# Kernel tuning notes

Hardware: AMD Instinct MI355X
Metric: run time of the kernel (lower is better)

The kernel has to match this reference:

```python
import jax, jax.numpy as jnp
import numpy as np

B, F, FO, J, H, IN, OUT = 256, 16, 32, 22, 8, 256, 512
HID = OUT // H    # 64
HS = HID // 2     # 32 (spatial/temporal half)
NEG = -1e9


def setup_inputs() -> dict:
    key = jax.random.key(0)
    ks = jax.random.split(key, 10)
    s = 0.02
    f32 = jnp.float32
    return {
        "q": jax.random.normal(ks[0], (B, FO, J, IN), f32),
        "k": jax.random.normal(ks[1], (B, F, J, IN), f32),
        "v": jax.random.normal(ks[2], (B, F, J, IN), f32),
        "mask_s": jax.random.randint(ks[3], (J, J), 0, 2, jnp.int32),
        "mask_t": jax.random.randint(ks[4], (FO, FO), 0, 2, jnp.int32),
        "Wq_w": jax.random.normal(ks[5], (IN, OUT), f32) * s,
        "Wq_b": jnp.zeros((OUT,), f32),
        "Wk_w": jax.random.normal(ks[6], (IN, OUT), f32) * s,
        "Wk_b": jnp.zeros((OUT,), f32),
        "Wv_w": jax.random.normal(ks[7], (IN, OUT), f32) * s,
        "Wv_b": jnp.zeros((OUT,), f32),
        "conv_s_w": jax.random.normal(ks[8], (FO, F), f32) * s,  # 1x1 Conv2d over frame channels
        "conv_s_b": jnp.zeros((FO,), f32),
        "conv_t_w": jax.random.normal(ks[9], (FO, F), f32) * s,
        "conv_t_b": jnp.zeros((FO,), f32),
    }


def _forward(q, k, v, mask_s, mask_t, Wq_w, Wq_b, Wk_w, Wk_b, Wv_w, Wv_b,
             conv_s_w, conv_s_b, conv_t_w, conv_t_b):
    b = q.shape[0]
    temporal_size = q.shape[1]  # torch: q.shape[1] AFTER Wq -> num_frames_out
    q = q @ Wq_w + Wq_b
    k = k @ Wk_w + Wk_b
    v = v @ Wv_w + Wv_b
    # raw reshapes, exactly as the torch module (not a standard head split)
    q = q.reshape(b, H, FO, J, HID)
    k = k.reshape(b, H, F, J, HID)
    v = v.reshape(b, H, F, J, HID)
    q_s, q_t = q[..., :HS], q[..., HS:]
    k_s, k_t = k[..., :HS], k[..., HS:]
    v_s, v_t = v[..., :HS], v[..., HS:]

    def explode_s(x):
        # (b,H,F,J,HS) -> merge heads into channels -> 1x1 conv over frames -> (b,H,FO,J,HS)
        x = x.transpose(0, 2, 3, 1, 4).reshape(b, F, J, H * HS)
        x = jnp.einsum('of,bfjc->bojc', conv_s_w, x) + conv_s_b[None, :, None, None]
        return x.reshape(b, FO, J, H, HS).transpose(0, 3, 1, 2, 4)

    k_s = explode_s(k_s)
    v_s = explode_s(v_s)

    q_t = q_t.transpose(0, 1, 3, 2, 4)  # (b,H,J,FO,HS)
    v_t = v_t.transpose(0, 1, 3, 2, 4)  # (b,H,J,F,HS)
    kt = k_t.reshape(b * H, F, J, HS)   # torch double-permute is identity
    kt = jnp.einsum('of,nfjc->nojc', conv_t_w, kt) + conv_t_b[None, :, None, None]
    k_t = kt.reshape(b, H, FO, J, HS).transpose(0, 1, 3, 2, 4)  # (b,H,J,FO,HS)

    # faithful to torch.einsum: no shared contraction index -> outer product of sums
    attn_s = jnp.einsum('bhtsc,bhtdu->bhtsu', q_s, jnp.swapaxes(k_s, 3, 4))  # (b,H,FO,J,J)
    attn_s = jnp.where(mask_s == 0, NEG, attn_s)
    attn_t = jnp.einsum('bhstf,bhsug->bhstg', q_t, jnp.swapaxes(k_t, 3, 4))  # (b,H,J,FO,FO)
    attn_t = jnp.where(mask_t == 0, NEG, attn_t)
    attn_s = jax.nn.softmax(attn_s, axis=-1)
    attn_t = jax.nn.softmax(attn_t, axis=-1)

    # 'bhtss' takes the diagonal over the two joint axes (torch semantics)
    x_s = jnp.einsum('bhtss,bhtuf->bhtsf', attn_s, v_s)          # (b,H,FO,J,HS)
    x_t = jnp.einsum('bhstf,bhsug->bhstg', attn_t, v_t)          # (b,H,J,FO,HS)
    x_t = x_t.transpose(0, 1, 3, 2, 4)                            # (b,H,FO,J,HS)

    x_up = jnp.concatenate([x_s[:, :, :temporal_size], x_t], axis=-1)
    x_after_s = x_s[:, :, temporal_size:]                         # empty when q covers FO frames
    x_after = jnp.concatenate([x_after_s, jnp.zeros_like(x_after_s)], axis=-1)
    x = jnp.concatenate([x_up, x_after], axis=2)
    x = x.transpose(0, 2, 3, 1, 4).reshape(b, FO, J, H * HID)
    return x


def reference(q, k, v, mask_s, mask_t, Wq_w, Wq_b, Wk_w, Wk_b, Wv_w, Wv_b,
              conv_s_w, conv_s_b, conv_t_w, conv_t_b):
    return _forward(q, k, v, mask_s, mask_t, Wq_w, Wq_b, Wk_w, Wk_b, Wv_w, Wv_b,
                    conv_s_w, conv_s_b, conv_t_w, conv_t_b)
```

## Files before the change

kernel.cpp:

```cpp
#include <hip/hip_runtime.h>


#define NEGV (-1000000000.0f)

typedef __attribute__((ext_vector_type(8))) short short8;
typedef __attribute__((ext_vector_type(4))) float f32x4;

__device__ inline ushort f2bf(float f) {
  union { float f; unsigned u; } a;
  a.f = f;
  unsigned u = a.u;
  return (ushort)((u + 0x7FFFu + ((u >> 16) & 1u)) >> 16);
}

#define PUTG(g, pa, pb)                                                        \
  {                                                                            \
    int row_ = (g) >> 5, gl_ = (g) & 31;                                       \
    int gp_ = gl_ ^ (row_ & 7);                                                \
    short8 u_;                                                                 \
    u_[0] = (short)f2bf(pa[0]); u_[1] = (short)f2bf(pa[1]);                    \
    u_[2] = (short)f2bf(pa[2]); u_[3] = (short)f2bf(pa[3]);                    \
    u_[4] = (short)f2bf(pb[0]); u_[5] = (short)f2bf(pb[1]);                    \
    u_[6] = (short)f2bf(pb[2]); u_[7] = (short)f2bf(pb[3]);                    \
    *reinterpret_cast<short8*>(&lA[row_ * 256 + gp_ * 8]) = u_;                \
  }

#define STAGE44_NT(SRCPTR)                                                     \
  {                                                                            \
    const float* vsrc_ = (SRCPTR);                                             \
    int g0 = tid, g1 = tid + 512, g2 = tid + 1024;                             \
    f32x4 a0 = __builtin_nontemporal_load(                                     \
        reinterpret_cast<const f32x4*>(vsrc_ + g0 * 8));                       \
    f32x4 b0 = __builtin_nontemporal_load(                                     \
        reinterpret_cast<const f32x4*>(vsrc_ + g0 * 8 + 4));                   \
    f32x4 a1 = __builtin_nontemporal_load(                                     \
        reinterpret_cast<const f32x4*>(vsrc_ + g1 * 8));                       \
    f32x4 b1 = __builtin_nontemporal_load(                                     \
        reinterpret_cast<const f32x4*>(vsrc_ + g1 * 8 + 4));                   \
    f32x4 a2 = {0, 0, 0, 0}, b2 = {0, 0, 0, 0};                                \
    if (g2 < 1408) {                                                           \
      a2 = __builtin_nontemporal_load(                                         \
          reinterpret_cast<const f32x4*>(vsrc_ + g2 * 8));                     \
      b2 = __builtin_nontemporal_load(                                         \
          reinterpret_cast<const f32x4*>(vsrc_ + g2 * 8 + 4));                 \
    }                                                                          \
    PUTG(g0, a0, b0);                                                          \
    PUTG(g1, a1, b1);                                                          \
    if (g2 < 1408) PUTG(g2, a2, b2);                                           \
    if (tid < 128) {                                                           \
      int g = 1408 + tid;                                                      \
      int row_ = g >> 5, gp_ = (g & 31) ^ (row_ & 7);                          \
      short8 z = {0, 0, 0, 0, 0, 0, 0, 0};                                     \
      *reinterpret_cast<short8*>(&lA[row_ * 256 + gp_ * 8]) = z;               \
    }                                                                          \
  }

__global__ __launch_bounds__(512) void prep_all_kernel(const float* __restrict__ Wq_w,
                                                       const float* __restrict__ Wq_b,
                                                       const float* __restrict__ Wk_w,
                                                       const float* __restrict__ Wk_b,
                                                       const float* __restrict__ Wv_w,
                                                       ushort* __restrict__ qwf,
                                                       ushort* __restrict__ kwf,
                                                       ushort* __restrict__ wvtf,
                                                       float* __restrict__ sqb,
                                                       float* __restrict__ skb) {
  int bx = blockIdx.x, tid = threadIdx.x;
  if (bx < 256) {
    int idx = bx * 512 + tid;
    int e = idx & 7;
    int lane = (idx >> 3) & 63;
    int ks = (idx >> 9) & 7;
    int nt = idx >> 12;
    int r0 = lane & 15, kb = lane >> 4;
    int k = ks * 32 + kb * 8 + e;
    int ch = nt * 16 + r0;
    wvtf[idx] = f2bf(Wv_w[k * 512 + ch]);
  } else if (bx < 272) {
    int idx = (bx - 256) * 512 + tid;
    int which = idx >> 12;
    int r = idx & 4095;
    int e = r & 7;
    int lane = (r >> 3) & 63;
    int ks = r >> 9;
    int m = lane & 15, kb = lane >> 4;
    int k = ks * 32 + kb * 8 + e;
    float s = 0.f;
    if (m < 8) {
      const float* W = which ? Wk_w : Wq_w;
      const float4* p = reinterpret_cast<const float4*>(W + (size_t)k * 512 + m * 64);
      #pragma unroll
      for (int c4 = 0; c4 < 8; ++c4) {
        float4 x = p[c4];
        s += x.x + x.y + x.z + x.w;
      }
    }
    (which ? kwf : qwf)[r] = f2bf(s);
  } else {
    if (tid < 8) {
      float s = 0.f;
      for (int c = 0; c < 32; ++c) s += Wq_b[tid * 64 + c];
      sqb[tid] = s;
    } else if (tid < 16) {
      int mm = tid - 8;
      float s = 0.f;
      for (int c = 0; c < 32; ++c) s += Wk_b[mm * 64 + c];
      skb[mm] = s;
    }
  }
}

__global__ __launch_bounds__(512, 2) void mega_kernel(const float* __restrict__ q,
                                                      const float* __restrict__ k,
                                                      const float* __restrict__ v,
                                                      const ushort* __restrict__ qwf,
                                                      const ushort* __restrict__ kwf,
                                                      const ushort* __restrict__ wvtf,
                                                      const float* __restrict__ sqb,
                                                      const float* __restrict__ skb,
                                                      const float* __restrict__ Wv_b,
                                                      const float* __restrict__ csw,
                                                      const float* __restrict__ csb,
                                                      const int* __restrict__ mask_s,
                                                      float* __restrict__ out) {
  int bh = blockIdx.x;
  int b = bh >> 3, h = bh & 7;
  __shared__ float sbuf[6656];
  __shared__ float qs[32][23];
  __shared__ float kraw[16][23];
  __shared__ float vsg[16][33];
  __shared__ float vtl[22][33];
  __shared__ float lcsw[32][17];
  __shared__ int msk[484];
  ushort* lA = reinterpret_cast<ushort*>(sbuf);
  float* dump = sbuf;
  float* kssp = sbuf;
  float* vssp = sbuf + 736;
  float* dgp = sbuf + 1792;
  int tid = threadIdx.x, lane = tid & 63, w = tid >> 6;
  int r0 = lane & 15, kb = lane >> 4;

  STAGE44_NT(v + (size_t)bh * 11264);

  if (tid < 484) msk[tid] = mask_s[tid];
  {
    int t = tid >> 4, f = tid & 15;
    lcsw[t][f] = csw[t * 16 + f];
  }
  if (tid < 32) lcsw[tid][16] = csb[tid];

  const float* qbase = q + (size_t)(b * 704 + 4 * h * 22) * 256;
  const float* kbase = k + (size_t)(b * 352 + 2 * h * 22) * 256;
  for (int pass = 0; pass < 2; ++pass) {
    int u = pass == 0 ? w : 8;
    if (pass == 1 && w != 0) break;
    bool isK = u >= 6;
    int ut = isK ? u - 6 : u;
    int limit = isK ? 44 : 88;
    int rr = ut * 16 + r0;
    if (rr >= limit) rr = 0;
    const float* src = (isK ? kbase : qbase) + (size_t)rr * 256;
    const ushort* wf = isK ? kwf : qwf;
    f32x4 acc = {0.f, 0.f, 0.f, 0.f};
    #pragma unroll
    for (int ks = 0; ks < 8; ++ks) {
      f32x4 xa = __builtin_nontemporal_load(
          reinterpret_cast<const f32x4*>(src + ks * 32 + kb * 8));
      f32x4 xb = __builtin_nontemporal_load(
          reinterpret_cast<const f32x4*>(src + ks * 32 + kb * 8 + 4));
      short8 a;
      a[0] = (short)f2bf(xa[0]); a[1] = (short)f2bf(xa[1]);
      a[2] = (short)f2bf(xa[2]); a[3] = (short)f2bf(xa[3]);
      a[4] = (short)f2bf(xb[0]); a[5] = (short)f2bf(xb[1]);
      a[6] = (short)f2bf(xb[2]); a[7] = (short)f2bf(xb[3]);
      short8 bf = *reinterpret_cast<const short8*>(wf + (ks * 64 + lane) * 8);
      acc = __builtin_amdgcn_mfma_f32_16x16x32_bf16(a, bf, acc, 0, 0, 0);
    }
    if (r0 < 8) {
      int m = r0;
      float bias = isK ? skb[m] : sqb[m];
      #pragma unroll
      for (int reg = 0; reg < 4; ++reg) {
        int R = ut * 16 + kb * 4 + reg;
        if (R < limit) {
          if (!isK) {
            int fo2l = R / 22, j2 = R % 22;
            int lf = fo2l * 11264 + j2 * 512 + m * 64;
            int t = lf / 1408;
            int s = (lf % 1408) >> 6;
            qs[t][s] = acc[reg] + bias;
          } else {
            int f2l = R / 22, j2 = R % 22;
            int lf = f2l * 11264 + j2 * 512 + m * 64;
            int floc = lf / 1408;
            int jj = (lf % 1408) >> 6;
            kraw[floc][jj] = acc[reg] + bias;
          }
        }
      }
    }
  }
  __syncthreads();

  int nt0 = w * 4;
  f32x4 acc[3][4];
  #pragma unroll
  for (int m = 0; m < 3; ++m)
    #pragma unroll
    for (int n = 0; n < 4; ++n) acc[m][n] = (f32x4){0.f, 0.f, 0.f, 0.f};

  #pragma unroll
  for (int ks = 0; ks < 8; ++ks) {
    int go = ((ks * 4 + kb) ^ (r0 & 7)) * 8;
    short8 a0 = *reinterpret_cast<const short8*>(&lA[(r0) * 256 + go]);
    short8 a1 = *reinterpret_cast<const short8*>(&lA[(16 + r0) * 256 + go]);
    short8 a2 = *reinterpret_cast<const short8*>(&lA[(32 + r0) * 256 + go]);
    #pragma unroll
    for (int n = 0; n < 4; ++n) {
      short8 bf = *reinterpret_cast<const short8*>(
          wvtf + ((size_t)((nt0 + n) * 8 + ks) * 64 + lane) * 8);
      acc[0][n] = __builtin_amdgcn_mfma_f32_16x16x32_bf16(bf, a0, acc[0][n], 0, 0, 0);
      acc[1][n] = __builtin_amdgcn_mfma_f32_16x16x32_bf16(bf, a1, acc[1][n], 0, 0, 0);
      acc[2][n] = __builtin_amdgcn_mfma_f32_16x16x32_bf16(bf, a2, acc[2][n], 0, 0, 0);
    }
  }
  __syncthreads();

  #pragma unroll
  for (int n = 0; n < 4; ++n) {
    float4 bq = *reinterpret_cast<const float4*>(Wv_b + w * 64 + n * 16 + kb * 4);
    int dbase = tid * 13;
    #pragma unroll
    for (int m = 0; m < 3; ++m) {
      dump[dbase + m * 4 + 0] = acc[m][n][0] + bq.x;
      dump[dbase + m * 4 + 1] = acc[m][n][1] + bq.y;
      dump[dbase + m * 4 + 2] = acc[m][n][2] + bq.z;
      dump[dbase + m * 4 + 3] = acc[m][n][3] + bq.w;
    }
    __syncthreads();
    if (n < 2) {
      if (tid < 256) {
        int f = tid >> 4, rest = tid & 15;
        int kb2 = rest >> 2, reg = rest & 3;
        float s = 0.f;
        #pragma unroll
        for (int u = 0; u < 22; ++u) {
          int fj = f * 22 + u;
          int f2 = (fj >= 176) ? 1 : 0;
          int rem = fj - f2 * 176;
          int j = rem >> 3, ww = rem & 7;
          int vrow = f2 * 22 + j;
          int m = vrow >> 4, rr2 = vrow & 15;
          s += dump[(ww * 64 + kb2 * 16 + rr2) * 13 + m * 4 + reg];
        }
        vsg[f][n * 16 + kb2 * 4 + reg] = s;
      }
    } else {
      if (tid < 352) {
        int jj = tid >> 4, rest = tid & 15;
        int kb2 = rest >> 2, reg = rest & 3;
        float s = 0.f;
        #pragma unroll
        for (int f = 0; f < 16; ++f) {
          int fj = f * 22 + jj;
          int f2 = (fj >= 176) ? 1 : 0;
          int rem = fj - f2 * 176;
          int j = rem >> 3, ww = rem & 7;
          int vrow = f2 * 22 + j;
          int m = vrow >> 4, rr2 = vrow & 15;
          s += dump[(ww * 64 + kb2 * 16 + rr2) * 13 + m * 4 + reg];
        }
        vtl[jj][(n - 2) * 16 + kb2 * 4 + reg] = s;
      }
    }
    __syncthreads();
  }

  float* ob = out + (size_t)b * 32 * 22 * 512 + h * 64;
  for (int i = tid; i < 5632; i += 512) {
    int ts = i >> 3, w4 = i & 7;
    int t = ts / 22, s = ts % 22;
    int d0 = 32 + w4 * 4;
    const float* tp = &vtl[s][d0 - 32];
    f32x4 val = {tp[0], tp[1], tp[2], tp[3]};
    *reinterpret_cast<f32x4*>(ob + (size_t)(t * 22 + s) * 512 + d0) = val;
  }

  for (int o = tid; o < 704; o += 512) {
    int t = o / 22, j = o % 22;
    float a = 32.0f * lcsw[t][16];
    #pragma unroll
    for (int f = 0; f < 16; ++f) a += lcsw[t][f] * kraw[f][j];
    kssp[t * 23 + j] = a;
  }
  {
    int t = tid >> 4, d2 = (tid & 15) * 2;
    float a0 = 22.0f * lcsw[t][16], a1 = a0;
    #pragma unroll
    for (int f = 0; f < 16; ++f) {
      float cw = lcsw[t][f];
      a0 += cw * vsg[f][d2];
      a1 += cw * vsg[f][d2 + 1];
    }
    vssp[t * 33 + d2] = a0;
    vssp[t * 33 + d2 + 1] = a1;
  }
  __syncthreads();

  for (int p = tid; p < 704; p += 512) {
    int t = p / 22, s = p % 22;
    float qv = qs[t][s];
    float mx = -3.0e38f;
    #pragma unroll
    for (int u = 0; u < 22; ++u) {
      float av = msk[s * 22 + u] ? qv * kssp[t * 23 + u] : NEGV;
      mx = fmaxf(mx, av);
    }
    float den = 0.f;
    #pragma unroll
    for (int u = 0; u < 22; ++u) {
      float av = msk[s * 22 + u] ? qv * kssp[t * 23 + u] : NEGV;
      den += expf(av - mx);
    }
    float as = msk[s * 22 + s] ? qv * kssp[t * 23 + s] : NEGV;
    dgp[t * 23 + s] = expf(as - mx) / den;
  }
  __syncthreads();

  for (int i = tid; i < 5632; i += 512) {
    int ts = i >> 3, w4 = i & 7;
    int t = ts / 22, s = ts % 22;
    int d0 = w4 * 4;
    float g = dgp[t * 23 + s];
    const float* vp = &vssp[t * 33 + d0];
    f32x4 val = {g * vp[0], g * vp[1], g * vp[2], g * vp[3]};
    *reinterpret_cast<f32x4*>(ob + (size_t)(t * 22 + s) * 512 + d0) = val;
  }
}

extern "C" void kernel_launch(void* const* d_in, const int* in_sizes, int n_in,
                              void* d_out, int out_size, void* d_ws, size_t ws_size,
                              hipStream_t stream) {
  const float* q = (const float*)d_in[0];
  const float* k = (const float*)d_in[1];
  const float* v = (const float*)d_in[2];
  const int* mask_s = (const int*)d_in[3];
  const float* Wq_w = (const float*)d_in[5];
  const float* Wq_b = (const float*)d_in[6];
  const float* Wk_w = (const float*)d_in[7];
  const float* Wk_b = (const float*)d_in[8];
  const float* Wv_w = (const float*)d_in[9];
  const float* Wv_b = (const float*)d_in[10];
  const float* csw = (const float*)d_in[11];
  const float* csb = (const float*)d_in[12];
  float* out = (float*)d_out;

  float* ws = (float*)d_ws;
  float* sqb = ws;
  float* skb = ws + 8;
  ushort* wvtf = (ushort*)(ws + 16);
  ushort* qwf = (ushort*)(ws + 65552);
  ushort* kwf = (ushort*)(ws + 67600);

  hipLaunchKernelGGL(prep_all_kernel, dim3(273), dim3(512), 0, stream,
                     Wq_w, Wq_b, Wk_w, Wk_b, Wv_w, qwf, kwf, wvtf, sqb, skb);
  hipLaunchKernelGGL(mega_kernel, dim3(2048), dim3(512), 0, stream,
                     q, k, v, qwf, kwf, wvtf, sqb, skb, Wv_b, csw, csb, mask_s, out);
}
```

Baseline: 187.7 us.

## Split V-projection MFMA into two column passes and restructure LDS reduction dump

```diff
diff --git a/kernel.cpp b/kernel.cpp
--- a/kernel.cpp
+++ b/kernel.cpp
@@ -125,24 +125,23 @@
                                                       float* __restrict__ out) {
   int bh = blockIdx.x;
   int b = bh >> 3, h = bh & 7;
-  __shared__ float sbuf[6656];
+  __shared__ ushort lA[48 * 256];
+  __shared__ float dmp[4096];
   __shared__ float qs[32][23];
   __shared__ float kraw[16][23];
   __shared__ float vsg[16][33];
   __shared__ float vtl[22][33];
   __shared__ float lcsw[32][17];
-  __shared__ int msk[484];
-  ushort* lA = reinterpret_cast<ushort*>(sbuf);
-  float* dump = sbuf;
-  float* kssp = sbuf;
-  float* vssp = sbuf + 736;
-  float* dgp = sbuf + 1792;
+  __shared__ char msk[484];
+  float* kssp = dmp;
+  float* vssp = dmp + 736;
+  float* dgp = dmp + 1792;
   int tid = threadIdx.x, lane = tid & 63, w = tid >> 6;
   int r0 = lane & 15, kb = lane >> 4;
 
   STAGE44_NT(v + (size_t)bh * 11264);
 
-  if (tid < 484) msk[tid] = mask_s[tid];
+  if (tid < 484) msk[tid] = (char)mask_s[tid];
   {
     int t = tid >> 4, f = tid & 15;
     lcsw[t][f] = csw[t * 16 + f];
@@ -203,78 +202,105 @@
   __syncthreads();
 
   int nt0 = w * 4;
-  f32x4 acc[3][4];
   #pragma unroll
-  for (int m = 0; m < 3; ++m)
-    #pragma unroll
-    for (int n = 0; n < 4; ++n) acc[m][n] = (f32x4){0.f, 0.f, 0.f, 0.f};
-
-  #pragma unroll
-  for (int ks = 0; ks < 8; ++ks) {
-    int go = ((ks * 4 + kb) ^ (r0 & 7)) * 8;
-    short8 a0 = *reinterpret_cast<const short8*>(&lA[(r0) * 256 + go]);
-    short8 a1 = *reinterpret_cast<const short8*>(&lA[(16 + r0) * 256 + go]);
-    short8 a2 = *reinterpret_cast<const short8*>(&lA[(32 + r0) * 256 + go]);
-    #pragma unroll
-    for (int n = 0; n < 4; ++n) {
-      short8 bf = *reinterpret_cast<const short8*>(
-          wvtf + ((size_t)((nt0 + n) * 8 + ks) * 64 + lane) * 8);
-      acc[0][n] = __builtin_amdgcn_mfma_f32_16x16x32_bf16(bf, a0, acc[0][n], 0, 0, 0);
-      acc[1][n] = __builtin_amdgcn_mfma_f32_16x16x32_bf16(bf, a1, acc[1][n], 0, 0, 0);
-      acc[2][n] = __builtin_amdgcn_mfma_f32_16x16x32_bf16(bf, a2, acc[2][n], 0, 0, 0);
+  for (int r = 0; r < 2; ++r) {
+    f32x4 acc[3][2];
+    #pragma unroll
+    for (int m = 0; m < 3; ++m)
+      #pragma unroll
+      for (int nl = 0; nl < 2; ++nl) acc[m][nl] = (f32x4){0.f, 0.f, 0.f, 0.f};
+
+    #pragma unroll
+    for (int ks = 0; ks < 8; ++ks) {
+      int go = ((ks * 4 + kb) ^ (r0 & 7)) * 8;
+      short8 a0 = *reinterpret_cast<const short8*>(&lA[(r0) * 256 + go]);
+      short8 a1 = *reinterpret_cast<const short8*>(&lA[(16 + r0) * 256 + go]);
+      short8 a2 = *reinterpret_cast<const short8*>(&lA[(32 + r0) * 256 + go]);
+      #pragma unroll
+      for (int nl = 0; nl < 2; ++nl) {
+        short8 bf = *reinterpret_cast<const short8*>(
+            wvtf + ((size_t)((nt0 + r * 2 + nl) * 8 + ks) * 64 + lane) * 8);
+        acc[0][nl] = __builtin_amdgcn_mfma_f32_16x16x32_bf16(bf, a0, acc[0][nl], 0, 0, 0);
+        acc[1][nl] = __builtin_amdgcn_mfma_f32_16x16x32_bf16(bf, a1, acc[1][nl], 0, 0, 0);
+        acc[2][nl] = __builtin_amdgcn_mfma_f32_16x16x32_bf16(bf, a2, acc[2][nl], 0, 0, 0);
+      }
+    }
+
+    #pragma unroll
+    for (int nl = 0; nl < 2; ++nl) {
+      int n = r * 2 + nl;
+      float4 bq = *reinterpret_cast<const float4*>(Wv_b + w * 64 + n * 16 + kb * 4);
+      #pragma unroll
+      for (int msub = 0; msub < 2; ++msub) {
+        __syncthreads();
+        if (msub == 0) {
+          #pragma unroll
+          for (int m = 0; m < 2; ++m) {
+            dmp[(m * 4 + 0) * 512 + tid] = acc[m][nl][0] + bq.x;
+            dmp[(m * 4 + 1) * 512 + tid] = acc[m][nl][1] + bq.y;
+            dmp[(m * 4 + 2) * 512 + tid] = acc[m][nl][2] + bq.z;
+            dmp[(m * 4 + 3) * 512 + tid] = acc[m][nl][3] + bq.w;
+          }
+        } else {
+          dmp[0 * 512 + tid] = acc[2][nl][0] + bq.x;
+          dmp[1 * 512 + tid] = acc[2][nl][1] + bq.y;
+          dmp[2 * 512 + tid] = acc[2][nl][2] + bq.z;
+          dmp[3 * 512 + tid] = acc[2][nl][3] + bq.w;
+        }
+        __syncthreads();
+        if (n < 2) {
+          if (tid < 256) {
+            int f = tid >> 4, rest = tid & 15;
+            int kb2 = rest >> 2, reg = rest & 3;
+            float s = 0.f;
+            #pragma unroll
+            for (int u = 0; u < 22; ++u) {
+              int fj = f * 22 + u;
+              int f2 = (fj >= 176) ? 1 : 0;
+              int rem = fj - f2 * 176;
+              int j = rem >> 3, ww = rem & 7;
+              int vrow = f2 * 22 + j;
+              int m = vrow >> 4, rr2 = vrow & 15;
+              int src = ww * 64 + kb2 * 16 + rr2;
+              if (msub == 0) {
+                if (m < 2) s += dmp[(m * 4 + reg) * 512 + src];
+              } else {
+                if (m == 2) s += dmp[reg * 512 + src];
+              }
+            }
+            int d = n * 16 + kb2 * 4 + reg;
+            if (msub == 0) vsg[f][d] = s;
+            else vsg[f][d] += s;
+          }
+        } else {
+          if (tid < 352) {
+            int jj = tid >> 4, rest = tid & 15;
+            int kb2 = rest >> 2, reg = rest & 3;
+            float s = 0.f;
+            #pragma unroll
+            for (int f = 0; f < 16; ++f) {
+              int fj = f * 22 + jj;
+              int f2 = (fj >= 176) ? 1 : 0;
+              int rem = fj - f2 * 176;
+              int j = rem >> 3, ww = rem & 7;
+              int vrow = f2 * 22 + j;
+              int m = vrow >> 4, rr2 = vrow & 15;
+              int src = ww * 64 + kb2 * 16 + rr2;
+              if (msub == 0) {
+                if (m < 2) s += dmp[(m * 4 + reg) * 512 + src];
+              } else {
+                if (m == 2) s += dmp[reg * 512 + src];
+              }
+            }
+            int g = (n - 2) * 16 + kb2 * 4 + reg;
+            if (msub == 0) vtl[jj][g] = s;
+            else vtl[jj][g] += s;
+          }
+        }
+      }
     }
   }
   __syncthreads();
-
-  #pragma unroll
-  for (int n = 0; n < 4; ++n) {
-    float4 bq = *reinterpret_cast<const float4*>(Wv_b + w * 64 + n * 16 + kb * 4);
-    int dbase = tid * 13;
-    #pragma unroll
-    for (int m = 0; m < 3; ++m) {
-      dump[dbase + m * 4 + 0] = acc[m][n][0] + bq.x;
-      dump[dbase + m * 4 + 1] = acc[m][n][1] + bq.y;
-      dump[dbase + m * 4 + 2] = acc[m][n][2] + bq.z;
-      dump[dbase + m * 4 + 3] = acc[m][n][3] + bq.w;
-    }
-    __syncthreads();
-    if (n < 2) {
-      if (tid < 256) {
-        int f = tid >> 4, rest = tid & 15;
-        int kb2 = rest >> 2, reg = rest & 3;
-        float s = 0.f;
-        #pragma unroll
-        for (int u = 0; u < 22; ++u) {
-          int fj = f * 22 + u;
-          int f2 = (fj >= 176) ? 1 : 0;
-          int rem = fj - f2 * 176;
-          int j = rem >> 3, ww = rem & 7;
-          int vrow = f2 * 22 + j;
-          int m = vrow >> 4, rr2 = vrow & 15;
-          s += dump[(ww * 64 + kb2 * 16 + rr2) * 13 + m * 4 + reg];
-        }
-        vsg[f][n * 16 + kb2 * 4 + reg] = s;
-      }
-    } else {
-      if (tid < 352) {
-        int jj = tid >> 4, rest = tid & 15;
-        int kb2 = rest >> 2, reg = rest & 3;
-        float s = 0.f;
-        #pragma unroll
-        for (int f = 0; f < 16; ++f) {
-          int fj = f * 22 + jj;
-          int f2 = (fj >= 176) ? 1 : 0;
-          int rem = fj - f2 * 176;
-          int j = rem >> 3, ww = rem & 7;
-          int vrow = f2 * 22 + j;
-          int m = vrow >> 4, rr2 = vrow & 15;
-          s += dump[(ww * 64 + kb2 * 16 + rr2) * 13 + m * 4 + reg];
-        }
-        vtl[jj][(n - 2) * 16 + kb2 * 4 + reg] = s;
-      }
-    }
-    __syncthreads();
-  }
 
   float* ob = out + (size_t)b * 32 * 22 * 512 + h * 64;
   for (int i = tid; i < 5632; i += 512) {
```

Result: slower. 226.6 us (+20.7%).
